# Kernel tuning notes

Hardware: AMD Instinct MI355X
Metric: run time of the kernel (lower is better)

The kernel has to match this reference:

```python
import jax, jax.numpy as jnp
import numpy as np

VOCAB, D, S, W, B = 32000, 768, 512, 300, 64
LMAX = 4  # max chars per word (spans are 1-3 chars)


def setup_inputs() -> dict:
    key = jax.random.key(0)
    k1, k2, k3, k4 = jax.random.split(key, 4)
    ernie_output = jax.random.normal(k1, (B, S, D), dtype=jnp.float32)
    word_embedding = jax.random.normal(k2, (VOCAB, D), dtype=jnp.float32)
    # structured word_index: (word_id, char_start, char_end) with contiguous spans
    lengths = jax.random.randint(k3, (B, W), 1, LMAX)  # 1..3 chars per word
    starts = 1 + jnp.concatenate(
        [jnp.zeros((B, 1), jnp.int32), jnp.cumsum(lengths, axis=1)[:, :-1]], axis=1
    ).astype(jnp.int32)
    ends = starts + lengths.astype(jnp.int32)  # tail words exceed S -> fallback path
    word_ids = jax.random.randint(k4, (B, W), 0, VOCAB, dtype=jnp.int32)
    word_index = jnp.stack([word_ids, starts, ends], axis=-1)  # (B, W, 3)
    return {"ernie_output": ernie_output, "word_embedding": word_embedding,
            "word_index": word_index}


def reference(ernie_output, word_embedding, word_index):
    Bb, Ss, Dd = ernie_output.shape
    Ww = word_index.shape[1]
    wid = word_index[..., 0]    # (B, W)
    st = word_index[..., 1]
    en = word_index[..., 2]
    span = en - st

    we = word_embedding[wid]                        # (B, W, D) query / fallback emb
    pos = st[..., None] + jnp.arange(LMAX)          # (B, W, LMAX)
    pos_c = jnp.clip(pos, 0, Ss - 1)
    chars = ernie_output[jnp.arange(Bb)[:, None, None], pos_c]  # (B, W, LMAX, D)

    # masked softmax attention pooling over the char span (len==1 reduces to copy)
    mask = jnp.arange(LMAX)[None, None, :] < jnp.maximum(span, 1)[..., None]
    scores = jnp.einsum('bwd,bwld->bwl', we, chars)
    scores = jnp.where(mask, scores, -jnp.inf)
    attn = jax.nn.softmax(scores, axis=-1)
    pooled = jnp.einsum('bwl,bwld->bwd', attn, chars)  # (B, W, D)

    in_range = en < Ss
    normal = jnp.where(in_range[..., None], pooled, we)

    # break semantics: first word with end<S and span<=0 fills positions j.. with
    # that word's embedding
    brk = in_range & (span <= 0)                   # (B, W)
    has_brk = jnp.any(brk, axis=1)
    first = jnp.where(has_brk, jnp.argmax(brk, axis=1), Ww)  # (B,)
    fill_id = wid[jnp.arange(Bb), jnp.clip(first, 0, Ww - 1)]
    fill = word_embedding[fill_id]                 # (B, D)
    jidx = jnp.arange(Ww)[None, :]
    out = jnp.where((jidx >= first[:, None])[..., None], fill[:, None, :], normal)
    return out
```

## Files before the change

kernel.cpp:

```cpp
#include <hip/hip_runtime.h>
#include <math.h>

#define VOCAB 32000
#define D 768
#define S 512
#define W 300
#define B 64
#define LMAX 4
#define GW 4
#define WGPB 75
#define MAXROWS 12
#define ROWB 3072

typedef float f32x4 __attribute__((ext_vector_type(4)));

__global__ __launch_bounds__(64) void find_first_kernel(
    const int* __restrict__ word_index,
    int* __restrict__ first_out,
    int* __restrict__ fill_id_out)
{
    const int b = blockIdx.x;
    const int lane = threadIdx.x;
    int my_first = W;
    for (int w = lane; w < W; w += 64) {
        const int base = (b * W + w) * 3;
        const int st = word_index[base + 1];
        const int en = word_index[base + 2];
        if (en < S && (en - st) <= 0) my_first = min(my_first, w);
    }
    #pragma unroll
    for (int off = 32; off > 0; off >>= 1)
        my_first = min(my_first, __shfl_xor(my_first, off));
    if (lane == 0) {
        first_out[b] = my_first;
        const int fw = min(my_first, W - 1);
        fill_id_out[b] = word_index[(b * W + fw) * 3 + 0];
    }
}

__device__ __forceinline__ float wave_bcast_sum(float p) {
    #pragma unroll
    for (int off = 32; off > 0; off >>= 1) p += __shfl_xor(p, off);
    return p;
}

__device__ __forceinline__ void async_copy16(const void* g, void* l) {
    __builtin_amdgcn_global_load_lds(
        (const __attribute__((address_space(1))) void*)g,
        (__attribute__((address_space(3))) void*)l,
        16, 0, 0);
}

__global__ __launch_bounds__(256) void pool_kernel(
    const float* __restrict__ ernie,
    const float* __restrict__ emb,
    const int*   __restrict__ word_index,
    const int*   __restrict__ first_arr,
    const int*   __restrict__ fill_arr,
    float* __restrict__ out)
{
    __shared__ __align__(16) char smem[MAXROWS * ROWB];

    const int blk = blockIdx.x;
    const int b   = blk / WGPB;
    const int wg  = blk - b * WGPB;
    const int w0  = wg * GW;
    const int lane   = threadIdx.x & 63;
    const int waveid = __builtin_amdgcn_readfirstlane(threadIdx.x >> 6);
    const int w      = w0 + waveid;
    const int gwave  = b * W + w;

    const int st0 = word_index[(b * W + w0) * 3 + 1];
    const int en3 = word_index[(b * W + w0 + GW - 1) * 3 + 2];
    int row_lo = max(min(st0, S), 0);
    int row_hi = min(en3, S);
    int nrows  = min(max(row_hi - row_lo, 0), MAXROWS);

    const int wid = word_index[gwave * 3 + 0];
    const int st  = word_index[gwave * 3 + 1];
    const int en  = word_index[gwave * 3 + 2];
    const int first = first_arr[b];
    const int rowid = (w >= first) ? fill_arr[b] : wid;

    const f32x4* wep = (const f32x4*)(emb + (size_t)rowid * D);
    f32x4 we0 = wep[lane], we1 = wep[lane + 64], we2 = wep[lane + 128];

    const char* gbase = (const char*)(ernie + ((size_t)b * S + row_lo) * D);
    const int nchunk = nrows * 3;
    for (int c = waveid; c < nchunk; c += 4)
        async_copy16(gbase + c * 1024 + lane * 16, smem + c * 1024);

    __syncthreads();

    f32x4* __restrict__ outp = (f32x4*)(out + (size_t)gwave * D);

    if (w >= first || en >= S) {
        __builtin_nontemporal_store(we0, &outp[lane]);
        __builtin_nontemporal_store(we1, &outp[lane + 64]);
        __builtin_nontemporal_store(we2, &outp[lane + 128]);
        return;
    }

    const int span_eff = min(max(en - st, 1), LMAX);
    const char* lbase = smem + (size_t)(st - row_lo) * ROWB;

    float m = -INFINITY, denom = 0.f;
    f32x4 acc0 = 0.f, acc1 = 0.f, acc2 = 0.f;

    #pragma unroll
    for (int l = 0; l < LMAX; ++l) {
        if (l >= span_eff) break;
        const f32x4* cp = (const f32x4*)(lbase + l * ROWB);
        f32x4 c0 = cp[lane];
        f32x4 c1 = cp[lane + 64];
        f32x4 c2 = cp[lane + 128];
        f32x4 pv = c0 * we0 + c1 * we1 + c2 * we2;
        float p = pv.x + pv.y + pv.z + pv.w;
        p = wave_bcast_sum(p);
        float mn = fmaxf(m, p);
        float scale = expf(m - mn);
        float e = expf(p - mn);
        denom = denom * scale + e;
        acc0 = acc0 * scale + e * c0;
        acc1 = acc1 * scale + e * c1;
        acc2 = acc2 * scale + e * c2;
        m = mn;
    }

    const float inv = 1.f / denom;
    __builtin_nontemporal_store(acc0 * inv, &outp[lane]);
    __builtin_nontemporal_store(acc1 * inv, &outp[lane + 64]);
    __builtin_nontemporal_store(acc2 * inv, &outp[lane + 128]);
}

extern "C" void kernel_launch(void* const* d_in, const int* in_sizes, int n_in,
                              void* d_out, int out_size, void* d_ws, size_t ws_size,
                              hipStream_t stream) {
    const float* ernie      = (const float*)d_in[0];
    const float* emb        = (const float*)d_in[1];
    const int*   word_index = (const int*)d_in[2];
    float* out = (float*)d_out;

    int* first_arr = (int*)d_ws;
    int* fill_arr  = first_arr + B;

    find_first_kernel<<<B, 64, 0, stream>>>(word_index, first_arr, fill_arr);

    const int grid = B * WGPB;
    pool_kernel<<<grid, 256, 0, stream>>>(ernie, emb, word_index,
                                          first_arr, fill_arr, out);
}
```

Measured before the change: 228.9 us.

## Make pool kernel persistent with double-buffered LDS prefetch of next group

The pool kernel becomes a persistent grid of 512 blocks, each looping over word groups with a stride of 512. While one group is computed, the next group's character rows are loaded asynchronously into a second LDS buffer, along with that group's query embeddings. The goal is to hide global-load latency behind the softmax pooling and to cut the cost of launching many short blocks. The trade-off is twice the LDS per block and fewer resident blocks per CU, which may reduce latency hiding from occupancy.

```diff
diff --git a/kernel.cpp b/kernel.cpp
--- a/kernel.cpp
+++ b/kernel.cpp
@@ -8,9 +8,12 @@
 #define B 64
 #define LMAX 4
 #define GW 4
-#define WGPB 75
+#define GPB 75
+#define NGRP (B * GPB)
 #define MAXROWS 12
 #define ROWB 3072
+#define BUFB (MAXROWS * ROWB)
+#define NBLK 512
 
 typedef float f32x4 __attribute__((ext_vector_type(4)));
 
@@ -51,50 +54,53 @@
         16, 0, 0);
 }
 
-__global__ __launch_bounds__(256) void pool_kernel(
-    const float* __restrict__ ernie,
-    const float* __restrict__ emb,
-    const int*   __restrict__ word_index,
-    const int*   __restrict__ first_arr,
-    const int*   __restrict__ fill_arr,
-    float* __restrict__ out)
-{
-    __shared__ __align__(16) char smem[MAXROWS * ROWB];
-
-    const int blk = blockIdx.x;
-    const int b   = blk / WGPB;
-    const int wg  = blk - b * WGPB;
-    const int w0  = wg * GW;
-    const int lane   = threadIdx.x & 63;
-    const int waveid = __builtin_amdgcn_readfirstlane(threadIdx.x >> 6);
-    const int w      = w0 + waveid;
-    const int gwave  = b * W + w;
-
+
+__device__ __forceinline__ int stage_group(
+    const float* __restrict__ ernie, const int* __restrict__ word_index,
+    int g, char* __restrict__ buf, int waveid, int lane)
+{
+    const int b  = g / GPB;
+    const int w0 = (g - b * GPB) * GW;
     const int st0 = word_index[(b * W + w0) * 3 + 1];
     const int en3 = word_index[(b * W + w0 + GW - 1) * 3 + 2];
-    int row_lo = max(min(st0, S), 0);
-    int row_hi = min(en3, S);
-    int nrows  = min(max(row_hi - row_lo, 0), MAXROWS);
-
-    const int wid = word_index[gwave * 3 + 0];
-    const int st  = word_index[gwave * 3 + 1];
-    const int en  = word_index[gwave * 3 + 2];
-    const int first = first_arr[b];
-    const int rowid = (w >= first) ? fill_arr[b] : wid;
-
-    const f32x4* wep = (const f32x4*)(emb + (size_t)rowid * D);
-    f32x4 we0 = wep[lane], we1 = wep[lane + 64], we2 = wep[lane + 128];
-
+    const int row_lo = max(min(st0, S), 0);
+    const int row_hi = min(en3, S);
+    const int nrows  = min(max(row_hi - row_lo, 0), MAXROWS);
     const char* gbase = (const char*)(ernie + ((size_t)b * S + row_lo) * D);
     const int nchunk = nrows * 3;
-    for (int c = waveid; c < nchunk; c += 4)
-        async_copy16(gbase + c * 1024 + lane * 16, smem + c * 1024);
-
-    __syncthreads();
-
-    f32x4* __restrict__ outp = (f32x4*)(out + (size_t)gwave * D);
-
-    if (w >= first || en >= S) {
+    for (int c = waveid; c < nchunk; c += GW)
+        async_copy16(gbase + c * 1024 + lane * 16, buf + c * 1024);
+    return row_lo;
+}
+
+__device__ __forceinline__ void load_we(
+    int g, int waveid, int lane, const int* __restrict__ word_index,
+    const int* __restrict__ first_arr, const int* __restrict__ fill_arr,
+    const float* __restrict__ emb, f32x4& we0, f32x4& we1, f32x4& we2)
+{
+    const int b = g / GPB;
+    const int w = (g - b * GPB) * GW + waveid;
+    const int gword = b * W + w;
+    const int wid = word_index[gword * 3 + 0];
+    const int rowid = (w >= first_arr[b]) ? fill_arr[b] : wid;
+    const f32x4* wep = (const f32x4*)(emb + (size_t)rowid * D);
+    we0 = wep[lane]; we1 = wep[lane + 64]; we2 = wep[lane + 128];
+}
+
+__device__ __forceinline__ void compute_word(
+    int g, int waveid, int lane, const char* __restrict__ buf, int row_lo,
+    f32x4 we0, f32x4 we1, f32x4 we2,
+    const int* __restrict__ word_index, const int* __restrict__ first_arr,
+    float* __restrict__ out)
+{
+    const int b = g / GPB;
+    const int w = (g - b * GPB) * GW + waveid;
+    const int gword = b * W + w;
+    const int st = word_index[gword * 3 + 1];
+    const int en = word_index[gword * 3 + 2];
+    f32x4* __restrict__ outp = (f32x4*)(out + (size_t)gword * D);
+
+    if (w >= first_arr[b] || en >= S) {
         __builtin_nontemporal_store(we0, &outp[lane]);
         __builtin_nontemporal_store(we1, &outp[lane + 64]);
         __builtin_nontemporal_store(we2, &outp[lane + 128]);
@@ -102,7 +108,7 @@
     }
 
     const int span_eff = min(max(en - st, 1), LMAX);
-    const char* lbase = smem + (size_t)(st - row_lo) * ROWB;
+    const char* lbase = buf + (size_t)(st - row_lo) * ROWB;
 
     float m = -INFINITY, denom = 0.f;
     f32x4 acc0 = 0.f, acc1 = 0.f, acc2 = 0.f;
@@ -133,6 +139,55 @@
     __builtin_nontemporal_store(acc2 * inv, &outp[lane + 128]);
 }
 
+__global__ __launch_bounds__(256) void pool_kernel(
+    const float* __restrict__ ernie,
+    const float* __restrict__ emb,
+    const int*   __restrict__ word_index,
+    const int*   __restrict__ first_arr,
+    const int*   __restrict__ fill_arr,
+    float* __restrict__ out)
+{
+    __shared__ __align__(16) char smem[2][BUFB];
+
+    const int lane   = threadIdx.x & 63;
+    const int waveid = __builtin_amdgcn_readfirstlane(threadIdx.x >> 6);
+
+    int g = blockIdx.x;
+    int rowA = stage_group(ernie, word_index, g, smem[0], waveid, lane);
+    f32x4 aw0, aw1, aw2;
+    load_we(g, waveid, lane, word_index, first_arr, fill_arr, emb, aw0, aw1, aw2);
+    int rowB = 0;
+    f32x4 bw0, bw1, bw2;
+
+    for (;;) {
+        int gn = g + NBLK;
+        __syncthreads();
+        const bool hasN1 = (gn < NGRP);
+        if (hasN1) {
+            rowB = stage_group(ernie, word_index, gn, smem[1], waveid, lane);
+            load_we(gn, waveid, lane, word_index, first_arr, fill_arr, emb,
+                    bw0, bw1, bw2);
+        }
+        compute_word(g, waveid, lane, smem[0], rowA, aw0, aw1, aw2,
+                     word_index, first_arr, out);
+        if (!hasN1) return;
+        g = gn;
+
+        gn = g + NBLK;
+        __syncthreads();
+        const bool hasN2 = (gn < NGRP);
+        if (hasN2) {
+            rowA = stage_group(ernie, word_index, gn, smem[0], waveid, lane);
+            load_we(gn, waveid, lane, word_index, first_arr, fill_arr, emb,
+                    aw0, aw1, aw2);
+        }
+        compute_word(g, waveid, lane, smem[1], rowB, bw0, bw1, bw2,
+                     word_index, first_arr, out);
+        if (!hasN2) return;
+        g = gn;
+    }
+}
+
 extern "C" void kernel_launch(void* const* d_in, const int* in_sizes, int n_in,
                               void* d_out, int out_size, void* d_ws, size_t ws_size,
                               hipStream_t stream) {
@@ -146,7 +201,6 @@
 
     find_first_kernel<<<B, 64, 0, stream>>>(word_index, first_arr, fill_arr);
 
-    const int grid = B * WGPB;
-    pool_kernel<<<grid, 256, 0, stream>>>(ernie, emb, word_index,
+    pool_kernel<<<NBLK, 256, 0, stream>>>(ernie, emb, word_index,
                                           first_arr, fill_arr, out);
 }
```

New measurement: 233.3 us. About the same (+1.9%).
